# Performance work log

Measured on AMD Instinct MI355X. Metric: run time of the kernel, lower is better.

Reference implementation:

```python
import jax, jax.numpy as jnp
import numpy as np

H, BS, NB, R, K = 2048, 128, 44, 64, 8   # hidden, block_size, num_blocks, basis_rank, top_k
B, S = 4, 2048
I = NB * BS                               # intermediate size = 5632


def setup_inputs() -> dict:
    key = jax.random.key(0)
    ks = jax.random.split(key, 10)
    N = B * S
    return {
        "hidden_states": jax.random.normal(ks[0], (B, S, H), jnp.float32),
        "active_idx": jax.random.randint(ks[1], (N, K), 0, NB, jnp.int32),
        "active_score": jax.random.uniform(ks[2], (N, K), dtype=jnp.float32),
        "gate_w": jax.random.normal(ks[3], (I, H), jnp.float32) * 0.02,
        "up_w": jax.random.normal(ks[4], (I, H), jnp.float32) * 0.02,
        "down_w": jax.random.normal(ks[5], (H, I), jnp.float32) * 0.02,
        "enc_w": jax.random.normal(ks[6], (R, H), jnp.float32) * 0.02,
        "enc_b": jnp.zeros((R,), jnp.float32),
        "decoder": jax.random.normal(ks[7], (NB, R, BS), jnp.float32) * 0.02,
        "basis_bias": jnp.zeros((NB, BS), jnp.float32),
        "comp_bias": jnp.zeros((H,), jnp.float32),
        "scale": jnp.array(1.0, jnp.float32),
    }


def reference(hidden_states, active_idx, active_score, gate_w, up_w, down_w,
              enc_w, enc_b, decoder, basis_bias, comp_bias, scale):
    Bb, Ss, Hh = hidden_states.shape
    N = Bb * Ss
    x = hidden_states.reshape(N, Hh)                          # [N, H]

    # routing weights: softmax over selected block scores (all idx valid here),
    # scattered into a dense per-token per-block weight map (duplicates accumulate)
    w = jax.nn.softmax(active_score, axis=-1)                 # [N, K]
    block_w = jnp.zeros((N, NB), x.dtype).at[
        jnp.arange(N)[:, None], active_idx].add(w)            # [N, NB]

    # gated SiLU MLP intermediate over all blocks (dense equivalent of the
    # per-token block gather-compute)
    act = jax.nn.silu(x @ gate_w.T) * (x @ up_w.T)            # [N, I]

    # low-rank basis compensation: latent -> per-block block_size channels
    latent = jax.nn.silu(x @ enc_w.T + enc_b)                 # [N, R]
    comp = jnp.einsum('nr,brc->nbc', latent, decoder) + basis_bias  # [N, NB, BS]

    act_b = act.reshape(N, NB, BS) + scale * comp             # [N, NB, BS]
    weighted = (act_b * block_w[:, :, None]).reshape(N, I)    # mask+weight inactive blocks to 0

    out = weighted @ down_w.T + comp_bias                     # scatter back via down proj
    return out.reshape(Bb, Ss, Hh)
```

## Files before the change

### kernel.cpp

```cpp
#include <hip/hip_runtime.h>
#include <hip/hip_cooperative_groups.h>

namespace cg = cooperative_groups;

#define H_  2048
#define BS_ 128
#define NB_ 44
#define R_  64
#define K_  8
#define N_  8192
#define I_  5632
#define MT  64
#define TILES 32
#define DOWN_GRID 512
#define HC  512
#define MT2 128
#define TILES_GU 16
#define GRID_GU (8 * 6 * TILES_GU)

typedef __bf16 bf16x8 __attribute__((ext_vector_type(8)));
typedef float  f32x4  __attribute__((ext_vector_type(4)));

__device__ __forceinline__ unsigned short f2bf(float f) {
  unsigned int u = __float_as_uint(f);
  u = (u + 0x7FFFu + ((u >> 16) & 1u)) >> 16;
  return (unsigned short)u;
}
__device__ __forceinline__ bf16x8 ld8(const unsigned short* p) {
  uint4 v = *reinterpret_cast<const uint4*>(p);
  return __builtin_bit_cast(bf16x8, v);
}
__device__ __forceinline__ bf16x8 lds8(const char* p) {
  uint4 v = *reinterpret_cast<const uint4*>(p);
  return __builtin_bit_cast(bf16x8, v);
}
__device__ __forceinline__ void gl16(const void* g, void* l) {
  __builtin_amdgcn_global_load_lds(
      (const __attribute__((address_space(1))) char*)g,
      (__attribute__((address_space(3))) char*)l, 16, 0, 0);
}
#define WAIT_VM(n) do { asm volatile("s_waitcnt vmcnt(" #n ")" ::: "memory"); \
                        __builtin_amdgcn_sched_barrier(0); } while (0)
#define WAIT_LGKM0 do { asm volatile("s_waitcnt lgkmcnt(0)" ::: "memory"); \
                        __builtin_amdgcn_sched_barrier(0); } while (0)
#define SBAR __builtin_amdgcn_s_barrier()

__global__ void cvt_xgu(const float* __restrict__ x, const float* __restrict__ gw,
                        const float* __restrict__ uw, const float* __restrict__ ew,
                        const float* __restrict__ dw,
                        unsigned short* __restrict__ xb,
                        unsigned short* __restrict__ gwb,
                        unsigned short* __restrict__ uwb,
                        unsigned short* __restrict__ ewb,
                        unsigned short* __restrict__ dwb) {
  const int NX4 = N_ * H_ / 4;
  const int NG4 = I_ * H_ / 4;
  const int NE4 = R_ * H_ / 4;
  const int ND4 = H_ * I_ / 4;
  int total = NX4 + 2 * NG4 + NE4 + ND4;
  int stride = gridDim.x * blockDim.x;
  for (int i = blockIdx.x * blockDim.x + threadIdx.x; i < total; i += stride) {
    if (i < NX4 + 2 * NG4 + NE4) {
      const float4* s; ushort4* d; int j;
      if (i < NX4)                  { s = (const float4*)x;  d = (ushort4*)xb;  j = i; }
      else if (i < NX4 + NG4)       { s = (const float4*)gw; d = (ushort4*)gwb; j = i - NX4; }
      else if (i < NX4 + 2 * NG4)   { s = (const float4*)uw; d = (ushort4*)uwb; j = i - NX4 - NG4; }
      else                          { s = (const float4*)ew; d = (ushort4*)ewb; j = i - NX4 - 2 * NG4; }
      float4 v = s[j];
      ushort4 o; o.x = f2bf(v.x); o.y = f2bf(v.y); o.z = f2bf(v.z); o.w = f2bf(v.w);
      d[j] = o;
    } else {
      int j = i - (NX4 + 2 * NG4 + NE4);
      float4 v = ((const float4*)dw)[j];
      int flat = j * 4;
      int h = flat / I_;
      int rem = flat - h * I_;
      int b = rem >> 7, k = rem & 127;
      ushort4 o; o.x = f2bf(v.x); o.y = f2bf(v.y); o.z = f2bf(v.z); o.w = f2bf(v.w);
      *(ushort4*)(dwb + ((size_t)b * H_ + h) * BS_ + k) = o;
    }
  }
}

__global__ void cvt_dec(const float* __restrict__ dec, unsigned short* __restrict__ decb) {
  int i = blockIdx.x * 256 + threadIdx.x;
  if (i >= NB_ * BS_ * R_) return;
  int b = i >> 13;
  int rem = i & 8191;
  int c = rem >> 6, r = rem & 63;
  decb[i] = f2bf(dec[(b << 13) + r * BS_ + c]);
}

__global__ void zero_counts(int* __restrict__ counts) {
  if (threadIdx.x < NB_) counts[threadIdx.x] = 0;
}

__global__ void prep_kernel(const float* __restrict__ score,
                            const int* __restrict__ aidx,
                            float* __restrict__ w_buf,
                            int* __restrict__ counts) {
  __shared__ int hist[NB_];
  int tid = threadIdx.x;
  if (tid < NB_) hist[tid] = 0;
  __syncthreads();
  int n = blockIdx.x * 256 + tid;
  float s[K_];
  float m = -1e30f;
#pragma unroll
  for (int k = 0; k < K_; k++) { s[k] = score[n * K_ + k]; m = fmaxf(m, s[k]); }
  float sum = 0.f;
#pragma unroll
  for (int k = 0; k < K_; k++) { s[k] = __expf(s[k] - m); sum += s[k]; }
  float inv = 1.f / sum;
#pragma unroll
  for (int k = 0; k < K_; k++) {
    w_buf[n * K_ + k] = s[k] * inv;
    atomicAdd(&hist[aidx[n * K_ + k]], 1);
  }
  __syncthreads();
  if (tid < NB_) atomicAdd(&counts[tid], hist[tid]);
}

__global__ void scan_kernel(const int* __restrict__ counts,
                            int* __restrict__ offsets,
                            int* __restrict__ cursors) {
  if (threadIdx.x == 0) {
    int acc = 0;
    for (int b = 0; b < NB_; b++) { offsets[b] = acc; cursors[b] = acc; acc += counts[b]; }
    offsets[NB_] = acc;
  }
}

__global__ void fill_kernel(const int* __restrict__ aidx,
                            const float* __restrict__ w_buf,
                            int* __restrict__ cursors,
                            int* __restrict__ tok_list,
                            float* __restrict__ wt_list,
                            int* __restrict__ inv) {
  int n = blockIdx.x * 256 + threadIdx.x;
#pragma unroll
  for (int k = 0; k < K_; k++) {
    int b = aidx[n * K_ + k];
    int pos = atomicAdd(&cursors[b], 1);
    tok_list[pos] = n;
    wt_list[pos] = w_buf[n * K_ + k];
    inv[n * K_ + k] = pos;
  }
}

__global__ __launch_bounds__(256) void latent_mfma(
    const unsigned short* __restrict__ xb,
    const unsigned short* __restrict__ ewb,
    float* __restrict__ lat_part) {
  __shared__ __align__(16) char smem[16384];
  int tid = threadIdx.x;
  int wv = tid >> 6, lane = tid & 63;
  int lo = lane & 15, hi = lane >> 4;
  int grp = blockIdx.x >> 2, ksl = blockIdx.x & 3;
  int n0 = grp * 64;
  int k0 = ksl * 512;

  int rowA = tid >> 2;
  int jA = (tid & 3) ^ ((rowA >> 1) & 3);
  const unsigned short* srcA = xb + (size_t)(n0 + rowA) * H_ + k0 + jA * 8;
  const unsigned short* srcB = ewb + (size_t)rowA * H_ + k0 + jA * 8;

  gl16(srcA, smem + wv * 1024);
  gl16(srcB, smem + 8192 + wv * 1024);

  f32x4 acc[4] = {};
  int cur = 0;
  for (int ks = 0; ks < 512; ks += 32) {
    if (ks + 32 < 512) {
      gl16(srcA + ks + 32, smem + (cur ^ 1) * 4096 + wv * 1024);
      gl16(srcB + ks + 32, smem + 8192 + (cur ^ 1) * 4096 + wv * 1024);
      WAIT_VM(2);
    } else {
      WAIT_VM(0);
    }
    SBAR;
    int rB = wv * 16 + lo;
    bf16x8 Bf = lds8(smem + 8192 + cur * 4096 + (rB * 4 + (hi ^ ((rB >> 1) & 3))) * 16);
#pragma unroll
    for (int m = 0; m < 4; m++) {
      int row = m * 16 + lo;
      bf16x8 Af = lds8(smem + cur * 4096 + (row * 4 + (hi ^ ((row >> 1) & 3))) * 16);
      acc[m] = __builtin_amdgcn_mfma_f32_16x16x32_bf16(Af, Bf, acc[m], 0, 0, 0);
    }
    WAIT_LGKM0;
    SBAR;
    cur ^= 1;
  }

  int r = wv * 16 + lo;
  float* dst = lat_part + (size_t)ksl * N_ * R_;
#pragma unroll
  for (int m = 0; m < 4; m++) {
#pragma unroll
    for (int rg = 0; rg < 4; rg++) {
      int tok = n0 + m * 16 + hi * 4 + rg;
      dst[(size_t)tok * R_ + r] = acc[m][rg];
    }
  }
}

__global__ void latent_combine(const float* __restrict__ lp,
                               const float* __restrict__ enc_b,
                               unsigned short* __restrict__ lat) {
  const int T = N_ * R_;
  int i = blockIdx.x * 256 + threadIdx.x;
  if (i >= T) return;
  float v = lp[i] + lp[T + i] + lp[2 * T + i] + lp[3 * T + i] + enc_b[i & (R_ - 1)];
  lat[i] = f2bf(v / (1.f + __expf(-v)));
}

__device__ __forceinline__ bool decode_bt(int p, int& b, int& tile) {
  b = (p & 7) + 8 * ((p >> 3) / TILES);
  tile = (p >> 3) % TILES;
  return b < NB_;
}
__device__ __forceinline__ bool decode_bt_gu(int p, int& b, int& tile) {
  b = (p & 7) + 8 * ((p >> 3) / TILES_GU);
  tile = (p >> 3) % TILES_GU;
  return b < NB_;
}

__global__ __launch_bounds__(512, 4) void gateup_kernel(
    const unsigned short* __restrict__ xb,
    const unsigned short* __restrict__ gwb,
    const unsigned short* __restrict__ uwb,
    const unsigned short* __restrict__ latb,
    const unsigned short* __restrict__ decb_all,
    const float* __restrict__ bbias,
    const float* __restrict__ scale_p,
    const int* __restrict__ counts,
    const int* __restrict__ offsets,
    const int* __restrict__ tok_list,
    const float* __restrict__ wt_list,
    unsigned short* __restrict__ actw) {
  int b, tile;
  if (!decode_bt_gu(blockIdx.x, b, tile)) return;
  int cnt = counts[b];
  int base = tile * MT2;
  if (base >= cnt) return;
  int off = offsets[b];

  __shared__ __align__(16) char smem[49152];

  int tid = threadIdx.x;
  int wv = tid >> 6, lane = tid & 63;
  int lo = lane & 15, hi = lane >> 4;
  int wr = wv >> 2, wc = wv & 3;

  int rowA = tid >> 2;
  int jA = (tid & 3) ^ ((rowA >> 1) & 3);
  int tokA = tok_list[off + min(base + rowA, cnt - 1)];
  const unsigned short* srcA = xb + (size_t)tokA * H_ + jA * 8;

  const unsigned short* gb = gwb + (size_t)b * BS_ * H_;
  const unsigned short* ub = uwb + (size_t)b * BS_ * H_;
  int cS = tid >> 2;
  int jS = (tid & 3) ^ ((cS >> 1) & 3);
  const unsigned short* srcG = gb + (size_t)cS * H_ + jS * 8;
  const unsigned short* srcU = ub + (size_t)cS * H_ + jS * 8;

  f32x4 accG[4][2] = {};
  f32x4 accU[4][2] = {};

  gl16(srcA, smem + wv * 1024);
  gl16(srcG, smem + 16384 + wv * 1024);
  gl16(srcU, smem + 32768 + wv * 1024);

  for (int it = 0; it < 64; ++it) {
    int ks = it * 32;
    if (it < 63) {
      int nb_ = (it + 1) & 1;
      gl16(srcA + ks + 32, smem + nb_ * 8192 + wv * 1024);
      gl16(srcG + ks + 32, smem + 16384 + nb_ * 8192 + wv * 1024);
      gl16(srcU + ks + 32, smem + 32768 + nb_ * 8192 + wv * 1024);
      WAIT_VM(3);
    } else {
      WAIT_VM(0);
    }
    SBAR;
    int cur = it & 1;
    bf16x8 Af[4];
#pragma unroll
    for (int m = 0; m < 4; m++) {
      int row = wr * 64 + m * 16 + lo;
      int off16 = row * 4 + (hi ^ ((row >> 1) & 3));
      Af[m] = lds8(smem + cur * 8192 + off16 * 16);
    }
    bf16x8 Gf[2], Uf[2];
#pragma unroll
    for (int cf = 0; cf < 2; cf++) {
      int c = wc * 32 + cf * 16 + lo;
      int off16 = c * 4 + (hi ^ ((c >> 1) & 3));
      Gf[cf] = lds8(smem + 16384 + cur * 8192 + off16 * 16);
      Uf[cf] = lds8(smem + 32768 + cur * 8192 + off16 * 16);
    }
#pragma unroll
    for (int m = 0; m < 4; m++) {
#pragma unroll
      for (int cf = 0; cf < 2; cf++) {
        accG[m][cf] = __builtin_amdgcn_mfma_f32_16x16x32_bf16(Af[m], Gf[cf], accG[m][cf], 0, 0, 0);
        accU[m][cf] = __builtin_amdgcn_mfma_f32_16x16x32_bf16(Af[m], Uf[cf], accU[m][cf], 0, 0, 0);
      }
    }
    WAIT_LGKM0;
    SBAR;
  }

#pragma unroll
  for (int s = 0; s < 2; s++) {
    int o = s * 512 + tid;
    int r_ = o >> 3;
    int j = (o & 7) ^ (r_ & 7);
    int tokL = tok_list[off + min(base + r_, cnt - 1)];
    gl16(latb + (size_t)tokL * R_ + j * 8, smem + 32768 + s * 8192 + wv * 1024);
  }
  const unsigned short* decb = decb_all + (size_t)b * BS_ * R_;
#pragma unroll
  for (int s = 0; s < 2; s++) {
    int o = s * 512 + tid;
    int c = o >> 3;
    int j = (o & 7) ^ (c & 7);
    gl16(decb + (size_t)c * R_ + j * 8, smem + 16384 + s * 8192 + wv * 1024);
  }
  __syncthreads();

  f32x4 accC[4][2] = {};
#pragma unroll
  for (int kk = 0; kk < 2; kk++) {
    bf16x8 L[4];
#pragma unroll
    for (int m = 0; m < 4; m++) {
      int row = wr * 64 + m * 16 + lo;
      int off16 = row * 8 + ((kk * 4 + hi) ^ (row & 7));
      L[m] = lds8(smem + 32768 + off16 * 16);
    }
#pragma unroll
    for (int cf = 0; cf < 2; cf++) {
      int c = wc * 32 + cf * 16 + lo;
      int off16 = c * 8 + ((kk * 4 + hi) ^ (c & 7));
      bf16x8 D = lds8(smem + 16384 + off16 * 16);
#pragma unroll
      for (int m = 0; m < 4; m++)
        accC[m][cf] = __builtin_amdgcn_mfma_f32_16x16x32_bf16(L[m], D, accC[m][cf], 0, 0, 0);
    }
  }

  float scal = scale_p[0];
  int cc[2] = { wc * 32 + lo, wc * 32 + 16 + lo };
  float bbv[2] = { bbias[b * BS_ + cc[0]], bbias[b * BS_ + cc[1]] };
#pragma unroll
  for (int m = 0; m < 4; m++) {
#pragma unroll
    for (int r = 0; r < 4; r++) {
      int t = wr * 64 + m * 16 + hi * 4 + r;
      int g = base + t;
      if (g < cnt) {
        float wt = wt_list[off + g];
        unsigned short* dst = actw + (size_t)(off + g) * BS_;
#pragma unroll
        for (int cf = 0; cf < 2; cf++) {
          float gg = accG[m][cf][r];
          float uu = accU[m][cf][r];
          float act = (gg / (1.f + __expf(-gg))) * uu;
          dst[cc[cf]] = f2bf((act + scal * (accC[m][cf][r] + bbv[cf])) * wt);
        }
      }
    }
  }
}

__global__ __launch_bounds__(256) void downred_kernel(
    const unsigned short* __restrict__ actw,
    const unsigned short* __restrict__ dwb,
    const int* __restrict__ counts,
    const int* __restrict__ offsets,
    const int* __restrict__ inv,
    const float* __restrict__ cbias,
    unsigned short* __restrict__ partial,
    float* __restrict__ out) {
  cg::grid_group grid = cg::this_grid();
  __shared__ __align__(16) unsigned short a_lds[MT * BS_];
  __shared__ __align__(16) char b_lds[2][16384];
  int tid = threadIdx.x;
  int wv = tid >> 6, lane = tid & 63;
  int lo = lane & 15, hi = lane >> 4;
  int rs = tid >> 4;
  int jc = tid & 15;

  for (int c = 0; c < H_ / HC; c++) {
    int hc0 = c * HC;
    unsigned short* pchunk = partial + (size_t)c * 65536 * HC;

    for (int p = blockIdx.x; p < 8 * 6 * TILES; p += DOWN_GRID) {
      int b, tile;
      if (!decode_bt(p, b, tile)) continue;
      int cnt = counts[b];
      int base = tile * MT;
      if (base >= cnt) continue;
      int off = offsets[b];

      for (int i = tid; i < MT * BS_ / 8; i += 256) {
        int t = i >> 4, cb = i & 15;
        int g = base + t;
        uint4 v = make_uint4(0, 0, 0, 0);
        if (g < cnt) v = *(const uint4*)(actw + (size_t)(off + g) * BS_ + cb * 8);
        *(uint4*)(&a_lds[t * BS_ + ((cb ^ (t & 7)) << 3)]) = v;
      }
      __syncthreads();

      bf16x8 Bf[4][4];
#pragma unroll
      for (int kst = 0; kst < 4; kst++)
#pragma unroll
        for (int sf = 0; sf < 4; sf++) {
          int t = sf * 16 + lo, cb = kst * 4 + hi;
          Bf[kst][sf] = ld8(&a_lds[t * BS_ + ((cb ^ (t & 7)) << 3)]);
        }

      const unsigned short* db = dwb + (size_t)b * H_ * BS_;
      {
        const unsigned short* d0 = db + (size_t)hc0 * BS_;
#pragma unroll
        for (int s = 0; s < 4; s++) {
          int r = s * 16 + rs;
          int j = jc ^ (r & 15);
          gl16(d0 + (size_t)r * BS_ + j * 8, b_lds[0] + s * 4096 + wv * 1024);
        }
      }
      __syncthreads();

      int cur = 0;
      for (int it = 0; it < HC / 64; it++) {
        if (it + 1 < HC / 64) {
          const unsigned short* dn = db + (size_t)(hc0 + (it + 1) * 64) * BS_;
#pragma unroll
          for (int s = 0; s < 4; s++) {
            int r = s * 16 + rs;
            int j = jc ^ (r & 15);
            gl16(dn + (size_t)r * BS_ + j * 8, b_lds[cur ^ 1] + s * 4096 + wv * 1024);
          }
        }
        f32x4 acc[4] = {};
        int rl = wv * 16 + lo;
#pragma unroll
        for (int kst = 0; kst < 4; kst++) {
          int cb = kst * 4 + hi;
          bf16x8 Aw = lds8(b_lds[cur] + (rl * 16 + (cb ^ lo)) * 16);
#pragma unroll
          for (int sf = 0; sf < 4; sf++)
            acc[sf] = __builtin_amdgcn_mfma_f32_16x16x32_bf16(Aw, Bf[kst][sf], acc[sf], 0, 0, 0);
        }
        int hrel = it * 64 + wv * 16 + hi * 4;
#pragma unroll
        for (int sf = 0; sf < 4; sf++) {
          int g = base + sf * 16 + lo;
          if (g < cnt) {
            uint2 pk;
            pk.x = (unsigned int)f2bf(acc[sf][0]) | ((unsigned int)f2bf(acc[sf][1]) << 16);
            pk.y = (unsigned int)f2bf(acc[sf][2]) | ((unsigned int)f2bf(acc[sf][3]) << 16);
            *(uint2*)(pchunk + (size_t)(off + g) * HC + hrel) = pk;
          }
        }
        __syncthreads();
        cur ^= 1;
      }
    }

    grid.sync();

    for (int n = blockIdx.x * 4 + wv; n < N_; n += DOWN_GRID * 4) {
      int rows[K_];
#pragma unroll
      for (int k = 0; k < K_; k++) rows[k] = inv[n * K_ + k];
      int cw = lane * 8;
      float a[8] = {0.f, 0.f, 0.f, 0.f, 0.f, 0.f, 0.f, 0.f};
#pragma unroll
      for (int k = 0; k < K_; k++) {
        uint4 v = *(const uint4*)(pchunk + (size_t)rows[k] * HC + cw);
        unsigned int w0 = v.x, w1 = v.y, w2 = v.z, w3 = v.w;
        a[0] += __uint_as_float(w0 << 16); a[1] += __uint_as_float(w0 & 0xFFFF0000u);
        a[2] += __uint_as_float(w1 << 16); a[3] += __uint_as_float(w1 & 0xFFFF0000u);
        a[4] += __uint_as_float(w2 << 16); a[5] += __uint_as_float(w2 & 0xFFFF0000u);
        a[6] += __uint_as_float(w3 << 16); a[7] += __uint_as_float(w3 & 0xFFFF0000u);
      }
      int h = hc0 + cw;
      float4 c0 = *(const float4*)(cbias + h);
      float4 c1 = *(const float4*)(cbias + h + 4);
      float4 o0 = make_float4(a[0] + c0.x, a[1] + c0.y, a[2] + c0.z, a[3] + c0.w);
      float4 o1 = make_float4(a[4] + c1.x, a[5] + c1.y, a[6] + c1.z, a[7] + c1.w);
      *(float4*)(out + (size_t)n * H_ + h) = o0;
      *(float4*)(out + (size_t)n * H_ + h + 4) = o1;
    }

    grid.sync();
  }
}

__global__ __launch_bounds__(256) void down_kernel(
    const unsigned short* __restrict__ actw,
    const unsigned short* __restrict__ dwb,
    const int* __restrict__ counts,
    const int* __restrict__ offsets,
    unsigned short* __restrict__ partial,
    int hc0) {
  __shared__ __align__(16) unsigned short a_lds[MT * BS_];
  __shared__ __align__(16) char b_lds[2][16384];
  int tid = threadIdx.x;
  int wv = tid >> 6, lane = tid & 63;
  int lo = lane & 15, hi = lane >> 4;
  int rs = tid >> 4;
  int jc = tid & 15;

  for (int p = blockIdx.x; p < 8 * 6 * TILES; p += DOWN_GRID) {
    int b, tile;
    if (!decode_bt(p, b, tile)) continue;
    int cnt = counts[b];
    int base = tile * MT;
    if (base >= cnt) continue;
    int off = offsets[b];

    for (int i = tid; i < MT * BS_ / 8; i += 256) {
      int t = i >> 4, cb = i & 15;
      int g = base + t;
      uint4 v = make_uint4(0, 0, 0, 0);
      if (g < cnt) v = *(const uint4*)(actw + (size_t)(off + g) * BS_ + cb * 8);
      *(uint4*)(&a_lds[t * BS_ + ((cb ^ (t & 7)) << 3)]) = v;
    }
    __syncthreads();

    bf16x8 Bf[4][4];
#pragma unroll
    for (int kst = 0; kst < 4; kst++)
#pragma unroll
      for (int sf = 0; sf < 4; sf++) {
        int t = sf * 16 + lo, cb = kst * 4 + hi;
        Bf[kst][sf] = ld8(&a_lds[t * BS_ + ((cb ^ (t & 7)) << 3)]);
      }

    const unsigned short* db = dwb + (size_t)b * H_ * BS_;
    {
      const unsigned short* d0 = db + (size_t)hc0 * BS_;
#pragma unroll
      for (int s = 0; s < 4; s++) {
        int r = s * 16 + rs;
        int j = jc ^ (r & 15);
        gl16(d0 + (size_t)r * BS_ + j * 8, b_lds[0] + s * 4096 + wv * 1024);
      }
    }
    __syncthreads();

    int cur = 0;
    for (int it = 0; it < HC / 64; it++) {
      if (it + 1 < HC / 64) {
        const unsigned short* dn = db + (size_t)(hc0 + (it + 1) * 64) * BS_;
#pragma unroll
        for (int s = 0; s < 4; s++) {
          int r = s * 16 + rs;
          int j = jc ^ (r & 15);
          gl16(dn + (size_t)r * BS_ + j * 8, b_lds[cur ^ 1] + s * 4096 + wv * 1024);
        }
      }
      f32x4 acc[4] = {};
      int rl = wv * 16 + lo;
#pragma unroll
      for (int kst = 0; kst < 4; kst++) {
        int cb = kst * 4 + hi;
        bf16x8 Aw = lds8(b_lds[cur] + (rl * 16 + (cb ^ lo)) * 16);
#pragma unroll
        for (int sf = 0; sf < 4; sf++)
          acc[sf] = __builtin_amdgcn_mfma_f32_16x16x32_bf16(Aw, Bf[kst][sf], acc[sf], 0, 0, 0);
      }
      int hrel = it * 64 + wv * 16 + hi * 4;
#pragma unroll
      for (int sf = 0; sf < 4; sf++) {
        int g = base + sf * 16 + lo;
        if (g < cnt) {
          uint2 pk;
          pk.x = (unsigned int)f2bf(acc[sf][0]) | ((unsigned int)f2bf(acc[sf][1]) << 16);
          pk.y = (unsigned int)f2bf(acc[sf][2]) | ((unsigned int)f2bf(acc[sf][3]) << 16);
          *(uint2*)(partial + (size_t)(off + g) * HC + hrel) = pk;
        }
      }
      __syncthreads();
      cur ^= 1;
    }
  }
}

__global__ __launch_bounds__(256) void reduce_kernel(
    const unsigned short* __restrict__ partial,
    const int* __restrict__ inv,
    const float* __restrict__ cbias,
    float* __restrict__ out, int hc0) {
  int wv = threadIdx.x >> 6, l = threadIdx.x & 63;
  int n = blockIdx.x * 4 + wv;
  int rows[K_];
#pragma unroll
  for (int k = 0; k < K_; k++) rows[k] = inv[n * K_ + k];
  int cw = l * 8;
  float a[8] = {0.f, 0.f, 0.f, 0.f, 0.f, 0.f, 0.f, 0.f};
#pragma unroll
  for (int k = 0; k < K_; k++) {
    uint4 v = *(const uint4*)(partial + (size_t)rows[k] * HC + cw);
    unsigned int w0 = v.x, w1 = v.y, w2 = v.z, w3 = v.w;
    a[0] += __uint_as_float(w0 << 16); a[1] += __uint_as_float(w0 & 0xFFFF0000u);
    a[2] += __uint_as_float(w1 << 16); a[3] += __uint_as_float(w1 & 0xFFFF0000u);
    a[4] += __uint_as_float(w2 << 16); a[5] += __uint_as_float(w2 & 0xFFFF0000u);
    a[6] += __uint_as_float(w3 << 16); a[7] += __uint_as_float(w3 & 0xFFFF0000u);
  }
  int h = hc0 + cw;
  float4 c0 = *(const float4*)(cbias + h);
  float4 c1 = *(const float4*)(cbias + h + 4);
  float4 o0 = make_float4(a[0] + c0.x, a[1] + c0.y, a[2] + c0.z, a[3] + c0.w);
  float4 o1 = make_float4(a[4] + c1.x, a[5] + c1.y, a[6] + c1.z, a[7] + c1.w);
  *(float4*)(out + (size_t)n * H_ + h) = o0;
  *(float4*)(out + (size_t)n * H_ + h + 4) = o1;
}

extern "C" void kernel_launch(void* const* d_in, const int* in_sizes, int n_in,
                              void* d_out, int out_size, void* d_ws, size_t ws_size,
                              hipStream_t stream) {
  const float* x       = (const float*)d_in[0];
  const int*   aidx    = (const int*)d_in[1];
  const float* score   = (const float*)d_in[2];
  const float* gate_w  = (const float*)d_in[3];
  const float* up_w    = (const float*)d_in[4];
  const float* down_w  = (const float*)d_in[5];
  const float* enc_w   = (const float*)d_in[6];
  const float* enc_b   = (const float*)d_in[7];
  const float* decoder = (const float*)d_in[8];
  const float* bbias   = (const float*)d_in[9];
  const float* cbias   = (const float*)d_in[10];
  const float* scale   = (const float*)d_in[11];
  float* out = (float*)d_out;

  char* ws = (char*)d_ws;
  const size_t OFF_GWB  = 33554432ull;
  const size_t OFF_UWB  = 56623104ull;
  const size_t OFF_DEC  = 79691776ull;
  const size_t OFF_LATB = 80412672ull;
  const size_t OFF_ENCB = 81461248ull;
  const size_t OFF_WBUF = 81723392ull;
  const size_t OFF_TOK  = 81985536ull;
  const size_t OFF_WT   = 82247680ull;
  const size_t OFF_INV  = 82509824ull;
  const size_t OFF_CNT  = 82771968ull;
  const size_t OFF_ACTW = 82772992ull;
  const size_t BASE_END = 99550208ull;
  const size_t DWB_SZ   = 23068672ull;
  const size_t PART_FULL = 268435456ull;

  unsigned short* xb   = (unsigned short*)(ws);
  unsigned short* gwb  = (unsigned short*)(ws + OFF_GWB);
  unsigned short* uwb  = (unsigned short*)(ws + OFF_UWB);
  unsigned short* decb = (unsigned short*)(ws + OFF_DEC);
  unsigned short* latb = (unsigned short*)(ws + OFF_LATB);
  unsigned short* ewb  = (unsigned short*)(ws + OFF_ENCB);
  float* w_buf         = (float*)(ws + OFF_WBUF);
  int*   tok_list      = (int*)(ws + OFF_TOK);
  float* wt_list       = (float*)(ws + OFF_WT);
  int*   inv           = (int*)(ws + OFF_INV);
  int*   counts        = (int*)(ws + OFF_CNT);
  int*   offsets       = counts + 64;
  int*   cursors       = counts + 128;
  unsigned short* actw = (unsigned short*)(ws + OFF_ACTW);

  unsigned short* dwb     = (unsigned short*)(ws + BASE_END);
  unsigned short* partial = (unsigned short*)(ws + BASE_END + DWB_SZ);
  float* lat_part         = (float*)(ws + BASE_END + DWB_SZ);

  bool full = ws_size >= BASE_END + DWB_SZ + PART_FULL;

  cvt_xgu<<<2048, 256, 0, stream>>>(x, gate_w, up_w, enc_w, down_w,
                                    xb, gwb, uwb, ewb, dwb);
  cvt_dec<<<(NB_ * BS_ * R_ + 255) / 256, 256, 0, stream>>>(decoder, decb);
  zero_counts<<<1, 64, 0, stream>>>(counts);
  prep_kernel<<<N_ / 256, 256, 0, stream>>>(score, aidx, w_buf, counts);
  scan_kernel<<<1, 64, 0, stream>>>(counts, offsets, cursors);
  fill_kernel<<<N_ / 256, 256, 0, stream>>>(aidx, w_buf, cursors, tok_list, wt_list, inv);
  latent_mfma<<<N_ / 16, 256, 0, stream>>>(xb, ewb, lat_part);
  latent_combine<<<N_ * R_ / 256, 256, 0, stream>>>(lat_part, enc_b, latb);
  gateup_kernel<<<GRID_GU, 512, 0, stream>>>(xb, gwb, uwb, latb, decb, bbias, scale,
                                             counts, offsets, tok_list, wt_list, actw);

  bool coop_done = false;
  if (full) {
    void* args[] = { (void*)&actw, (void*)&dwb, (void*)&counts, (void*)&offsets,
                     (void*)&inv, (void*)&cbias, (void*)&partial, (void*)&out };
    hipError_t rc = hipLaunchCooperativeKernel((const void*)downred_kernel,
                                               dim3(DOWN_GRID), dim3(256),
                                               args, 0, stream);
    coop_done = (rc == hipSuccess);
  }
  if (!coop_done) {
    for (int c = 0; c < H_ / HC; c++) {
      down_kernel<<<DOWN_GRID, 256, 0, stream>>>(actw, dwb, counts, offsets, partial, c * HC);
      reduce_kernel<<<N_ / 4, 256, 0, stream>>>(partial, inv, cbias, out, c * HC);
    }
  }
}
```

Measured before the change: 538.3 us.

## Fuse front-end conversion, routing, latent and gate-up into one cooperative kernel

Replaces the chain of small launches (conversion, prep, scan, fill, latent matmul plus combine, gate-up) with a single cooperative kernel that uses grid.sync between phases. The latent matmul now does its full K reduction per block with the bias and SiLU fused in, so the split-K partial buffer and the combine kernel go away. This removes launch overhead and intermediate round trips. The price is that the grid is limited to GRID_GU blocks of 512 threads with 48KB of LDS, which may lower parallelism in the conversion phase and cost occupancy. The old launch sequence is kept as a fallback if the cooperative launch fails.

```diff
diff --git a/kernel.cpp b/kernel.cpp
--- a/kernel.cpp
+++ b/kernel.cpp
@@ -17,6 +17,7 @@
 #define MT2 128
 #define TILES_GU 16
 #define GRID_GU (8 * 6 * TILES_GU)
+#define FRONT_GRID GRID_GU
 
 typedef __bf16 bf16x8 __attribute__((ext_vector_type(8)));
 typedef float  f32x4  __attribute__((ext_vector_type(4)));
@@ -44,6 +45,425 @@
 #define WAIT_LGKM0 do { asm volatile("s_waitcnt lgkmcnt(0)" ::: "memory"); \
                         __builtin_amdgcn_sched_barrier(0); } while (0)
 #define SBAR __builtin_amdgcn_s_barrier()
+
+__device__ __forceinline__ bool decode_bt(int p, int& b, int& tile) {
+  b = (p & 7) + 8 * ((p >> 3) / TILES);
+  tile = (p >> 3) % TILES;
+  return b < NB_;
+}
+__device__ __forceinline__ bool decode_bt_gu(int p, int& b, int& tile) {
+  b = (p & 7) + 8 * ((p >> 3) / TILES_GU);
+  tile = (p >> 3) % TILES_GU;
+  return b < NB_;
+}
+
+__global__ __launch_bounds__(512, 6) void front_kernel(
+    const float* __restrict__ x, const float* __restrict__ gw,
+    const float* __restrict__ uw, const float* __restrict__ ew,
+    const float* __restrict__ dw, const float* __restrict__ dec,
+    const float* __restrict__ score, const int* __restrict__ aidx,
+    const float* __restrict__ enc_b, const float* __restrict__ bbias,
+    const float* __restrict__ scale_p,
+    unsigned short* __restrict__ xb, unsigned short* __restrict__ gwb,
+    unsigned short* __restrict__ uwb, unsigned short* __restrict__ ewb,
+    unsigned short* __restrict__ dwb, unsigned short* __restrict__ decb_all,
+    unsigned short* __restrict__ latb,
+    float* __restrict__ w_buf, int* __restrict__ counts,
+    int* __restrict__ offsets, int* __restrict__ cursors,
+    int* __restrict__ tok_list, float* __restrict__ wt_list,
+    int* __restrict__ inv, unsigned short* __restrict__ actw) {
+  cg::grid_group grid = cg::this_grid();
+  __shared__ __align__(16) char smem[49152];
+  int tid = threadIdx.x;
+  int bId = blockIdx.x;
+
+  if (bId < 16) {
+    int* hist = (int*)smem;
+    if (tid < NB_) hist[tid] = 0;
+    __syncthreads();
+    int n = bId * 512 + tid;
+    float s[K_];
+    float m = -1e30f;
+#pragma unroll
+    for (int k = 0; k < K_; k++) { s[k] = score[n * K_ + k]; m = fmaxf(m, s[k]); }
+    float sum = 0.f;
+#pragma unroll
+    for (int k = 0; k < K_; k++) { s[k] = __expf(s[k] - m); sum += s[k]; }
+    float is = 1.f / sum;
+#pragma unroll
+    for (int k = 0; k < K_; k++) {
+      w_buf[n * K_ + k] = s[k] * is;
+      atomicAdd(&hist[aidx[n * K_ + k]], 1);
+    }
+    __syncthreads();
+    if (tid < NB_) atomicAdd(&counts[tid], hist[tid]);
+  }
+
+  {
+    const int NX4 = N_ * H_ / 4;
+    const int NG4 = I_ * H_ / 4;
+    const int NE4 = R_ * H_ / 4;
+    const int ND4 = H_ * I_ / 4;
+    int total = NX4 + 2 * NG4 + NE4 + ND4;
+    int stride = FRONT_GRID * 512;
+    for (int i = bId * 512 + tid; i < total; i += stride) {
+      if (i < NX4 + 2 * NG4 + NE4) {
+        const float4* s; ushort4* d; int j;
+        if (i < NX4)                { s = (const float4*)x;  d = (ushort4*)xb;  j = i; }
+        else if (i < NX4 + NG4)     { s = (const float4*)gw; d = (ushort4*)gwb; j = i - NX4; }
+        else if (i < NX4 + 2 * NG4) { s = (const float4*)uw; d = (ushort4*)uwb; j = i - NX4 - NG4; }
+        else                        { s = (const float4*)ew; d = (ushort4*)ewb; j = i - NX4 - 2 * NG4; }
+        float4 v = s[j];
+        ushort4 o; o.x = f2bf(v.x); o.y = f2bf(v.y); o.z = f2bf(v.z); o.w = f2bf(v.w);
+        d[j] = o;
+      } else {
+        int j = i - (NX4 + 2 * NG4 + NE4);
+        float4 v = ((const float4*)dw)[j];
+        int flat = j * 4;
+        int h = flat / I_;
+        int rem = flat - h * I_;
+        int b = rem >> 7, k = rem & 127;
+        ushort4 o; o.x = f2bf(v.x); o.y = f2bf(v.y); o.z = f2bf(v.z); o.w = f2bf(v.w);
+        *(ushort4*)(dwb + ((size_t)b * H_ + h) * BS_ + k) = o;
+      }
+    }
+    for (int i = bId * 512 + tid; i < NB_ * BS_ * R_; i += stride) {
+      int b = i >> 13;
+      int rem = i & 8191;
+      int c = rem >> 6, r = rem & 63;
+      decb_all[i] = f2bf(dec[(b << 13) + r * BS_ + c]);
+    }
+  }
+  grid.sync();
+
+  if (bId == 0 && tid == 0) {
+    int acc = 0;
+    for (int b = 0; b < NB_; b++) { offsets[b] = acc; cursors[b] = acc; acc += counts[b]; }
+    offsets[NB_] = acc;
+  }
+  grid.sync();
+
+  if (bId < 16) {
+    int n = bId * 512 + tid;
+#pragma unroll
+    for (int k = 0; k < K_; k++) {
+      int b = aidx[n * K_ + k];
+      int pos = atomicAdd(&cursors[b], 1);
+      tok_list[pos] = n;
+      wt_list[pos] = w_buf[n * K_ + k];
+      inv[n * K_ + k] = pos;
+    }
+  } else if (bId < 80) {
+    int g = tid >> 8;
+    int t = tid & 255;
+    int wvg = t >> 6;
+    int lane = t & 63, lo = lane & 15, hi = lane >> 4;
+    int n0 = (bId - 16) * 128 + g * 64;
+    char* sm = smem + g * 16384;
+    int rowA = t >> 2;
+    int jA = (t & 3) ^ ((rowA >> 1) & 3);
+    const unsigned short* srcA = xb + (size_t)(n0 + rowA) * H_ + jA * 8;
+    const unsigned short* srcB = ewb + (size_t)rowA * H_ + jA * 8;
+    gl16(srcA, sm + wvg * 1024);
+    gl16(srcB, sm + 8192 + wvg * 1024);
+    f32x4 acc[4] = {};
+    int cur = 0;
+    for (int ks = 0; ks < H_; ks += 32) {
+      if (ks + 32 < H_) {
+        gl16(srcA + ks + 32, sm + (cur ^ 1) * 4096 + wvg * 1024);
+        gl16(srcB + ks + 32, sm + 8192 + (cur ^ 1) * 4096 + wvg * 1024);
+        WAIT_VM(2);
+      } else {
+        WAIT_VM(0);
+      }
+      SBAR;
+      int rB = wvg * 16 + lo;
+      bf16x8 Bf = lds8(sm + 8192 + cur * 4096 + (rB * 4 + (hi ^ ((rB >> 1) & 3))) * 16);
+#pragma unroll
+      for (int m = 0; m < 4; m++) {
+        int row = m * 16 + lo;
+        bf16x8 Af = lds8(sm + cur * 4096 + (row * 4 + (hi ^ ((row >> 1) & 3))) * 16);
+        acc[m] = __builtin_amdgcn_mfma_f32_16x16x32_bf16(Af, Bf, acc[m], 0, 0, 0);
+      }
+      WAIT_LGKM0;
+      SBAR;
+      cur ^= 1;
+    }
+    int r = wvg * 16 + lo;
+    float eb = enc_b[r];
+#pragma unroll
+    for (int m = 0; m < 4; m++) {
+#pragma unroll
+      for (int rg = 0; rg < 4; rg++) {
+        int tok = n0 + m * 16 + hi * 4 + rg;
+        float v = acc[m][rg] + eb;
+        latb[(size_t)tok * R_ + r] = f2bf(v / (1.f + __expf(-v)));
+      }
+    }
+  }
+  grid.sync();
+
+  {
+    int b, tile;
+    if (!decode_bt_gu(bId, b, tile)) return;
+    int cnt = counts[b];
+    int base = tile * MT2;
+    if (base >= cnt) return;
+    int off = offsets[b];
+
+    int wv = tid >> 6, lane = tid & 63;
+    int lo = lane & 15, hi = lane >> 4;
+    int wr = wv >> 2, wc = wv & 3;
+
+    int rowA = tid >> 2;
+    int jA = (tid & 3) ^ ((rowA >> 1) & 3);
+    int tokA = tok_list[off + min(base + rowA, cnt - 1)];
+    const unsigned short* srcA = xb + (size_t)tokA * H_ + jA * 8;
+
+    const unsigned short* gb = gwb + (size_t)b * BS_ * H_;
+    const unsigned short* ub = uwb + (size_t)b * BS_ * H_;
+    int cS = tid >> 2;
+    int jS = (tid & 3) ^ ((cS >> 1) & 3);
+    const unsigned short* srcG = gb + (size_t)cS * H_ + jS * 8;
+    const unsigned short* srcU = ub + (size_t)cS * H_ + jS * 8;
+
+    f32x4 accG[4][2] = {};
+    f32x4 accU[4][2] = {};
+
+    gl16(srcA, smem + wv * 1024);
+    gl16(srcG, smem + 16384 + wv * 1024);
+    gl16(srcU, smem + 32768 + wv * 1024);
+
+    for (int it = 0; it < 64; ++it) {
+      int ks = it * 32;
+      if (it < 63) {
+        int nb_ = (it + 1) & 1;
+        gl16(srcA + ks + 32, smem + nb_ * 8192 + wv * 1024);
+        gl16(srcG + ks + 32, smem + 16384 + nb_ * 8192 + wv * 1024);
+        gl16(srcU + ks + 32, smem + 32768 + nb_ * 8192 + wv * 1024);
+        WAIT_VM(3);
+      } else {
+        WAIT_VM(0);
+      }
+      SBAR;
+      int cur = it & 1;
+      bf16x8 Af[4];
+#pragma unroll
+      for (int m = 0; m < 4; m++) {
+        int row = wr * 64 + m * 16 + lo;
+        int off16 = row * 4 + (hi ^ ((row >> 1) & 3));
+        Af[m] = lds8(smem + cur * 8192 + off16 * 16);
+      }
+      bf16x8 Gf[2], Uf[2];
+#pragma unroll
+      for (int cf = 0; cf < 2; cf++) {
+        int c = wc * 32 + cf * 16 + lo;
+        int off16 = c * 4 + (hi ^ ((c >> 1) & 3));
+        Gf[cf] = lds8(smem + 16384 + cur * 8192 + off16 * 16);
+        Uf[cf] = lds8(smem + 32768 + cur * 8192 + off16 * 16);
+      }
+#pragma unroll
+      for (int m = 0; m < 4; m++) {
+#pragma unroll
+        for (int cf = 0; cf < 2; cf++) {
+          accG[m][cf] = __builtin_amdgcn_mfma_f32_16x16x32_bf16(Af[m], Gf[cf], accG[m][cf], 0, 0, 0);
+          accU[m][cf] = __builtin_amdgcn_mfma_f32_16x16x32_bf16(Af[m], Uf[cf], accU[m][cf], 0, 0, 0);
+        }
+      }
+      WAIT_LGKM0;
+      SBAR;
+    }
+
+#pragma unroll
+    for (int s = 0; s < 2; s++) {
+      int o = s * 512 + tid;
+      int r_ = o >> 3;
+      int j = (o & 7) ^ (r_ & 7);
+      int tokL = tok_list[off + min(base + r_, cnt - 1)];
+      gl16(latb + (size_t)tokL * R_ + j * 8, smem + 32768 + s * 8192 + wv * 1024);
+    }
+    const unsigned short* decb = decb_all + (size_t)b * BS_ * R_;
+#pragma unroll
+    for (int s = 0; s < 2; s++) {
+      int o = s * 512 + tid;
+      int c = o >> 3;
+      int j = (o & 7) ^ (c & 7);
+      gl16(decb + (size_t)c * R_ + j * 8, smem + 16384 + s * 8192 + wv * 1024);
+    }
+    __syncthreads();
+
+    f32x4 accC[4][2] = {};
+#pragma unroll
+    for (int kk = 0; kk < 2; kk++) {
+      bf16x8 L[4];
+#pragma unroll
+      for (int m = 0; m < 4; m++) {
+        int row = wr * 64 + m * 16 + lo;
+        int off16 = row * 8 + ((kk * 4 + hi) ^ (row & 7));
+        L[m] = lds8(smem + 32768 + off16 * 16);
+      }
+#pragma unroll
+      for (int cf = 0; cf < 2; cf++) {
+        int c = wc * 32 + cf * 16 + lo;
+        int off16 = c * 8 + ((kk * 4 + hi) ^ (c & 7));
+        bf16x8 D = lds8(smem + 16384 + off16 * 16);
+#pragma unroll
+        for (int m = 0; m < 4; m++)
+          accC[m][cf] = __builtin_amdgcn_mfma_f32_16x16x32_bf16(L[m], D, accC[m][cf], 0, 0, 0);
+      }
+    }
+
+    float scal = scale_p[0];
+    int cc[2] = { wc * 32 + lo, wc * 32 + 16 + lo };
+    float bbv[2] = { bbias[b * BS_ + cc[0]], bbias[b * BS_ + cc[1]] };
+#pragma unroll
+    for (int m = 0; m < 4; m++) {
+#pragma unroll
+      for (int r = 0; r < 4; r++) {
+        int t = wr * 64 + m * 16 + hi * 4 + r;
+        int g = base + t;
+        if (g < cnt) {
+          float wt = wt_list[off + g];
+          unsigned short* dst = actw + (size_t)(off + g) * BS_;
+#pragma unroll
+          for (int cf = 0; cf < 2; cf++) {
+            float gg = accG[m][cf][r];
+            float uu = accU[m][cf][r];
+            float act = (gg / (1.f + __expf(-gg))) * uu;
+            dst[cc[cf]] = f2bf((act + scal * (accC[m][cf][r] + bbv[cf])) * wt);
+          }
+        }
+      }
+    }
+  }
+}
+
+__global__ __launch_bounds__(256) void downred_kernel(
+    const unsigned short* __restrict__ actw,
+    const unsigned short* __restrict__ dwb,
+    const int* __restrict__ counts,
+    const int* __restrict__ offsets,
+    const int* __restrict__ inv,
+    const float* __restrict__ cbias,
+    unsigned short* __restrict__ partial,
+    float* __restrict__ out) {
+  cg::grid_group grid = cg::this_grid();
+  __shared__ __align__(16) unsigned short a_lds[MT * BS_];
+  __shared__ __align__(16) char b_lds[2][16384];
+  int tid = threadIdx.x;
+  int wv = tid >> 6, lane = tid & 63;
+  int lo = lane & 15, hi = lane >> 4;
+  int rs = tid >> 4;
+  int jc = tid & 15;
+
+  for (int c = 0; c < H_ / HC; c++) {
+    int hc0 = c * HC;
+    unsigned short* pchunk = partial + (size_t)c * 65536 * HC;
+
+    for (int p = blockIdx.x; p < 8 * 6 * TILES; p += DOWN_GRID) {
+      int b, tile;
+      if (!decode_bt(p, b, tile)) continue;
+      int cnt = counts[b];
+      int base = tile * MT;
+      if (base >= cnt) continue;
+      int off = offsets[b];
+
+      for (int i = tid; i < MT * BS_ / 8; i += 256) {
+        int t = i >> 4, cb = i & 15;
+        int g = base + t;
+        uint4 v = make_uint4(0, 0, 0, 0);
+        if (g < cnt) v = *(const uint4*)(actw + (size_t)(off + g) * BS_ + cb * 8);
+        *(uint4*)(&a_lds[t * BS_ + ((cb ^ (t & 7)) << 3)]) = v;
+      }
+      __syncthreads();
+
+      bf16x8 Bf[4][4];
+#pragma unroll
+      for (int kst = 0; kst < 4; kst++)
+#pragma unroll
+        for (int sf = 0; sf < 4; sf++) {
+          int t = sf * 16 + lo, cb = kst * 4 + hi;
+          Bf[kst][sf] = ld8(&a_lds[t * BS_ + ((cb ^ (t & 7)) << 3)]);
+        }
+
+      const unsigned short* db = dwb + (size_t)b * H_ * BS_;
+      {
+        const unsigned short* d0 = db + (size_t)hc0 * BS_;
+#pragma unroll
+        for (int s = 0; s < 4; s++) {
+          int r = s * 16 + rs;
+          int j = jc ^ (r & 15);
+          gl16(d0 + (size_t)r * BS_ + j * 8, b_lds[0] + s * 4096 + wv * 1024);
+        }
+      }
+      __syncthreads();
+
+      int cur = 0;
+      for (int it = 0; it < HC / 64; it++) {
+        if (it + 1 < HC / 64) {
+          const unsigned short* dn = db + (size_t)(hc0 + (it + 1) * 64) * BS_;
+#pragma unroll
+          for (int s = 0; s < 4; s++) {
+            int r = s * 16 + rs;
+            int j = jc ^ (r & 15);
+            gl16(dn + (size_t)r * BS_ + j * 8, b_lds[cur ^ 1] + s * 4096 + wv * 1024);
+          }
+        }
+        f32x4 acc[4] = {};
+        int rl = wv * 16 + lo;
+#pragma unroll
+        for (int kst = 0; kst < 4; kst++) {
+          int cb = kst * 4 + hi;
+          bf16x8 Aw = lds8(b_lds[cur] + (rl * 16 + (cb ^ lo)) * 16);
+#pragma unroll
+          for (int sf = 0; sf < 4; sf++)
+            acc[sf] = __builtin_amdgcn_mfma_f32_16x16x32_bf16(Aw, Bf[kst][sf], acc[sf], 0, 0, 0);
+        }
+        int hrel = it * 64 + wv * 16 + hi * 4;
+#pragma unroll
+        for (int sf = 0; sf < 4; sf++) {
+          int g = base + sf * 16 + lo;
+          if (g < cnt) {
+            uint2 pk;
+            pk.x = (unsigned int)f2bf(acc[sf][0]) | ((unsigned int)f2bf(acc[sf][1]) << 16);
+            pk.y = (unsigned int)f2bf(acc[sf][2]) | ((unsigned int)f2bf(acc[sf][3]) << 16);
+            *(uint2*)(pchunk + (size_t)(off + g) * HC + hrel) = pk;
+          }
+        }
+        __syncthreads();
+        cur ^= 1;
+      }
+    }
+
+    grid.sync();
+
+    for (int n = blockIdx.x * 4 + wv; n < N_; n += DOWN_GRID * 4) {
+      int rows[K_];
+#pragma unroll
+      for (int k = 0; k < K_; k++) rows[k] = inv[n * K_ + k];
+      int cw = lane * 8;
+      float a[8] = {0.f, 0.f, 0.f, 0.f, 0.f, 0.f, 0.f, 0.f};
+#pragma unroll
+      for (int k = 0; k < K_; k++) {
+        uint4 v = *(const uint4*)(pchunk + (size_t)rows[k] * HC + cw);
+        unsigned int w0 = v.x, w1 = v.y, w2 = v.z, w3 = v.w;
+        a[0] += __uint_as_float(w0 << 16); a[1] += __uint_as_float(w0 & 0xFFFF0000u);
+        a[2] += __uint_as_float(w1 << 16); a[3] += __uint_as_float(w1 & 0xFFFF0000u);
+        a[4] += __uint_as_float(w2 << 16); a[5] += __uint_as_float(w2 & 0xFFFF0000u);
+        a[6] += __uint_as_float(w3 << 16); a[7] += __uint_as_float(w3 & 0xFFFF0000u);
+      }
+      int h = hc0 + cw;
+      float4 c0 = *(const float4*)(cbias + h);
+      float4 c1 = *(const float4*)(cbias + h + 4);
+      float4 o0 = make_float4(a[0] + c0.x, a[1] + c0.y, a[2] + c0.z, a[3] + c0.w);
+      float4 o1 = make_float4(a[4] + c1.x, a[5] + c1.y, a[6] + c1.z, a[7] + c1.w);
+      *(float4*)(out + (size_t)n * H_ + h) = o0;
+      *(float4*)(out + (size_t)n * H_ + h + 4) = o1;
+    }
+
+    grid.sync();
+  }
+}
 
 __global__ void cvt_xgu(const float* __restrict__ x, const float* __restrict__ gw,
                         const float* __restrict__ uw, const float* __restrict__ ew,
@@ -62,10 +482,10 @@
   for (int i = blockIdx.x * blockDim.x + threadIdx.x; i < total; i += stride) {
     if (i < NX4 + 2 * NG4 + NE4) {
       const float4* s; ushort4* d; int j;
-      if (i < NX4)                  { s = (const float4*)x;  d = (ushort4*)xb;  j = i; }
-      else if (i < NX4 + NG4)       { s = (const float4*)gw; d = (ushort4*)gwb; j = i - NX4; }
-      else if (i < NX4 + 2 * NG4)   { s = (const float4*)uw; d = (ushort4*)uwb; j = i - NX4 - NG4; }
-      else                          { s = (const float4*)ew; d = (ushort4*)ewb; j = i - NX4 - 2 * NG4; }
+      if (i < NX4)                { s = (const float4*)x;  d = (ushort4*)xb;  j = i; }
+      else if (i < NX4 + NG4)     { s = (const float4*)gw; d = (ushort4*)gwb; j = i - NX4; }
+      else if (i < NX4 + 2 * NG4) { s = (const float4*)uw; d = (ushort4*)uwb; j = i - NX4 - NG4; }
+      else                        { s = (const float4*)ew; d = (ushort4*)ewb; j = i - NX4 - 2 * NG4; }
       float4 v = s[j];
       ushort4 o; o.x = f2bf(v.x); o.y = f2bf(v.y); o.z = f2bf(v.z); o.w = f2bf(v.w);
       d[j] = o;
@@ -91,10 +511,6 @@
   decb[i] = f2bf(dec[(b << 13) + r * BS_ + c]);
 }
 
-__global__ void zero_counts(int* __restrict__ counts) {
-  if (threadIdx.x < NB_) counts[threadIdx.x] = 0;
-}
-
 __global__ void prep_kernel(const float* __restrict__ score,
                             const int* __restrict__ aidx,
                             float* __restrict__ w_buf,
@@ -111,10 +527,10 @@
   float sum = 0.f;
 #pragma unroll
   for (int k = 0; k < K_; k++) { s[k] = __expf(s[k] - m); sum += s[k]; }
-  float inv = 1.f / sum;
+  float is = 1.f / sum;
 #pragma unroll
   for (int k = 0; k < K_; k++) {
-    w_buf[n * K_ + k] = s[k] * inv;
+    w_buf[n * K_ + k] = s[k] * is;
     atomicAdd(&hist[aidx[n * K_ + k]], 1);
   }
   __syncthreads();
@@ -148,30 +564,29 @@
   }
 }
 
-__global__ __launch_bounds__(256) void latent_mfma(
+__global__ __launch_bounds__(256) void latent_fb(
     const unsigned short* __restrict__ xb,
     const unsigned short* __restrict__ ewb,
-    float* __restrict__ lat_part) {
+    const float* __restrict__ enc_b,
+    unsigned short* __restrict__ lat) {
   __shared__ __align__(16) char smem[16384];
   int tid = threadIdx.x;
   int wv = tid >> 6, lane = tid & 63;
   int lo = lane & 15, hi = lane >> 4;
-  int grp = blockIdx.x >> 2, ksl = blockIdx.x & 3;
-  int n0 = grp * 64;
-  int k0 = ksl * 512;
+  int n0 = blockIdx.x * 64;
 
   int rowA = tid >> 2;
   int jA = (tid & 3) ^ ((rowA >> 1) & 3);
-  const unsigned short* srcA = xb + (size_t)(n0 + rowA) * H_ + k0 + jA * 8;
-  const unsigned short* srcB = ewb + (size_t)rowA * H_ + k0 + jA * 8;
+  const unsigned short* srcA = xb + (size_t)(n0 + rowA) * H_ + jA * 8;
+  const unsigned short* srcB = ewb + (size_t)rowA * H_ + jA * 8;
 
   gl16(srcA, smem + wv * 1024);
   gl16(srcB, smem + 8192 + wv * 1024);
 
   f32x4 acc[4] = {};
   int cur = 0;
-  for (int ks = 0; ks < 512; ks += 32) {
-    if (ks + 32 < 512) {
+  for (int ks = 0; ks < H_; ks += 32) {
+    if (ks + 32 < H_) {
       gl16(srcA + ks + 32, smem + (cur ^ 1) * 4096 + wv * 1024);
       gl16(srcB + ks + 32, smem + 8192 + (cur ^ 1) * 4096 + wv * 1024);
       WAIT_VM(2);
@@ -193,36 +608,16 @@
   }
 
   int r = wv * 16 + lo;
-  float* dst = lat_part + (size_t)ksl * N_ * R_;
+  float eb = enc_b[r];
 #pragma unroll
   for (int m = 0; m < 4; m++) {
 #pragma unroll
     for (int rg = 0; rg < 4; rg++) {
       int tok = n0 + m * 16 + hi * 4 + rg;
-      dst[(size_t)tok * R_ + r] = acc[m][rg];
-    }
-  }
-}
-
-__global__ void latent_combine(const float* __restrict__ lp,
-                               const float* __restrict__ enc_b,
-                               unsigned short* __restrict__ lat) {
-  const int T = N_ * R_;
-  int i = blockIdx.x * 256 + threadIdx.x;
-  if (i >= T) return;
-  float v = lp[i] + lp[T + i] + lp[2 * T + i] + lp[3 * T + i] + enc_b[i & (R_ - 1)];
-  lat[i] = f2bf(v / (1.f + __expf(-v)));
-}
-
-__device__ __forceinline__ bool decode_bt(int p, int& b, int& tile) {
-  b = (p & 7) + 8 * ((p >> 3) / TILES);
-  tile = (p >> 3) % TILES;
-  return b < NB_;
-}
-__device__ __forceinline__ bool decode_bt_gu(int p, int& b, int& tile) {
-  b = (p & 7) + 8 * ((p >> 3) / TILES_GU);
-  tile = (p >> 3) % TILES_GU;
-  return b < NB_;
+      float v = acc[m][rg] + eb;
+      lat[(size_t)tok * R_ + r] = f2bf(v / (1.f + __expf(-v)));
+    }
+  }
 }
 
 __global__ __launch_bounds__(512, 4) void gateup_kernel(
@@ -374,133 +769,6 @@
   }
 }
 
-__global__ __launch_bounds__(256) void downred_kernel(
-    const unsigned short* __restrict__ actw,
-    const unsigned short* __restrict__ dwb,
-    const int* __restrict__ counts,
-    const int* __restrict__ offsets,
-    const int* __restrict__ inv,
-    const float* __restrict__ cbias,
-    unsigned short* __restrict__ partial,
-    float* __restrict__ out) {
-  cg::grid_group grid = cg::this_grid();
-  __shared__ __align__(16) unsigned short a_lds[MT * BS_];
-  __shared__ __align__(16) char b_lds[2][16384];
-  int tid = threadIdx.x;
-  int wv = tid >> 6, lane = tid & 63;
-  int lo = lane & 15, hi = lane >> 4;
-  int rs = tid >> 4;
-  int jc = tid & 15;
-
-  for (int c = 0; c < H_ / HC; c++) {
-    int hc0 = c * HC;
-    unsigned short* pchunk = partial + (size_t)c * 65536 * HC;
-
-    for (int p = blockIdx.x; p < 8 * 6 * TILES; p += DOWN_GRID) {
-      int b, tile;
-      if (!decode_bt(p, b, tile)) continue;
-      int cnt = counts[b];
-      int base = tile * MT;
-      if (base >= cnt) continue;
-      int off = offsets[b];
-
-      for (int i = tid; i < MT * BS_ / 8; i += 256) {
-        int t = i >> 4, cb = i & 15;
-        int g = base + t;
-        uint4 v = make_uint4(0, 0, 0, 0);
-        if (g < cnt) v = *(const uint4*)(actw + (size_t)(off + g) * BS_ + cb * 8);
-        *(uint4*)(&a_lds[t * BS_ + ((cb ^ (t & 7)) << 3)]) = v;
-      }
-      __syncthreads();
-
-      bf16x8 Bf[4][4];
-#pragma unroll
-      for (int kst = 0; kst < 4; kst++)
-#pragma unroll
-        for (int sf = 0; sf < 4; sf++) {
-          int t = sf * 16 + lo, cb = kst * 4 + hi;
-          Bf[kst][sf] = ld8(&a_lds[t * BS_ + ((cb ^ (t & 7)) << 3)]);
-        }
-
-      const unsigned short* db = dwb + (size_t)b * H_ * BS_;
-      {
-        const unsigned short* d0 = db + (size_t)hc0 * BS_;
-#pragma unroll
-        for (int s = 0; s < 4; s++) {
-          int r = s * 16 + rs;
-          int j = jc ^ (r & 15);
-          gl16(d0 + (size_t)r * BS_ + j * 8, b_lds[0] + s * 4096 + wv * 1024);
-        }
-      }
-      __syncthreads();
-
-      int cur = 0;
-      for (int it = 0; it < HC / 64; it++) {
-        if (it + 1 < HC / 64) {
-          const unsigned short* dn = db + (size_t)(hc0 + (it + 1) * 64) * BS_;
-#pragma unroll
-          for (int s = 0; s < 4; s++) {
-            int r = s * 16 + rs;
-            int j = jc ^ (r & 15);
-            gl16(dn + (size_t)r * BS_ + j * 8, b_lds[cur ^ 1] + s * 4096 + wv * 1024);
-          }
-        }
-        f32x4 acc[4] = {};
-        int rl = wv * 16 + lo;
-#pragma unroll
-        for (int kst = 0; kst < 4; kst++) {
-          int cb = kst * 4 + hi;
-          bf16x8 Aw = lds8(b_lds[cur] + (rl * 16 + (cb ^ lo)) * 16);
-#pragma unroll
-          for (int sf = 0; sf < 4; sf++)
-            acc[sf] = __builtin_amdgcn_mfma_f32_16x16x32_bf16(Aw, Bf[kst][sf], acc[sf], 0, 0, 0);
-        }
-        int hrel = it * 64 + wv * 16 + hi * 4;
-#pragma unroll
-        for (int sf = 0; sf < 4; sf++) {
-          int g = base + sf * 16 + lo;
-          if (g < cnt) {
-            uint2 pk;
-            pk.x = (unsigned int)f2bf(acc[sf][0]) | ((unsigned int)f2bf(acc[sf][1]) << 16);
-            pk.y = (unsigned int)f2bf(acc[sf][2]) | ((unsigned int)f2bf(acc[sf][3]) << 16);
-            *(uint2*)(pchunk + (size_t)(off + g) * HC + hrel) = pk;
-          }
-        }
-        __syncthreads();
-        cur ^= 1;
-      }
-    }
-
-    grid.sync();
-
-    for (int n = blockIdx.x * 4 + wv; n < N_; n += DOWN_GRID * 4) {
-      int rows[K_];
-#pragma unroll
-      for (int k = 0; k < K_; k++) rows[k] = inv[n * K_ + k];
-      int cw = lane * 8;
-      float a[8] = {0.f, 0.f, 0.f, 0.f, 0.f, 0.f, 0.f, 0.f};
-#pragma unroll
-      for (int k = 0; k < K_; k++) {
-        uint4 v = *(const uint4*)(pchunk + (size_t)rows[k] * HC + cw);
-        unsigned int w0 = v.x, w1 = v.y, w2 = v.z, w3 = v.w;
-        a[0] += __uint_as_float(w0 << 16); a[1] += __uint_as_float(w0 & 0xFFFF0000u);
-        a[2] += __uint_as_float(w1 << 16); a[3] += __uint_as_float(w1 & 0xFFFF0000u);
-        a[4] += __uint_as_float(w2 << 16); a[5] += __uint_as_float(w2 & 0xFFFF0000u);
-        a[6] += __uint_as_float(w3 << 16); a[7] += __uint_as_float(w3 & 0xFFFF0000u);
-      }
-      int h = hc0 + cw;
-      float4 c0 = *(const float4*)(cbias + h);
-      float4 c1 = *(const float4*)(cbias + h + 4);
-      float4 o0 = make_float4(a[0] + c0.x, a[1] + c0.y, a[2] + c0.z, a[3] + c0.w);
-      float4 o1 = make_float4(a[4] + c1.x, a[5] + c1.y, a[6] + c1.z, a[7] + c1.w);
-      *(float4*)(out + (size_t)n * H_ + h) = o0;
-      *(float4*)(out + (size_t)n * H_ + h + 4) = o1;
-    }
-
-    grid.sync();
-  }
-}
-
 __global__ __launch_bounds__(256) void down_kernel(
     const unsigned short* __restrict__ actw,
     const unsigned short* __restrict__ dwb,
@@ -672,21 +940,36 @@
 
   unsigned short* dwb     = (unsigned short*)(ws + BASE_END);
   unsigned short* partial = (unsigned short*)(ws + BASE_END + DWB_SZ);
-  float* lat_part         = (float*)(ws + BASE_END + DWB_SZ);
 
   bool full = ws_size >= BASE_END + DWB_SZ + PART_FULL;
 
-  cvt_xgu<<<2048, 256, 0, stream>>>(x, gate_w, up_w, enc_w, down_w,
-                                    xb, gwb, uwb, ewb, dwb);
-  cvt_dec<<<(NB_ * BS_ * R_ + 255) / 256, 256, 0, stream>>>(decoder, decb);
-  zero_counts<<<1, 64, 0, stream>>>(counts);
-  prep_kernel<<<N_ / 256, 256, 0, stream>>>(score, aidx, w_buf, counts);
-  scan_kernel<<<1, 64, 0, stream>>>(counts, offsets, cursors);
-  fill_kernel<<<N_ / 256, 256, 0, stream>>>(aidx, w_buf, cursors, tok_list, wt_list, inv);
-  latent_mfma<<<N_ / 16, 256, 0, stream>>>(xb, ewb, lat_part);
-  latent_combine<<<N_ * R_ / 256, 256, 0, stream>>>(lat_part, enc_b, latb);
-  gateup_kernel<<<GRID_GU, 512, 0, stream>>>(xb, gwb, uwb, latb, decb, bbias, scale,
-                                             counts, offsets, tok_list, wt_list, actw);
+  hipMemsetAsync(counts, 0, 64 * sizeof(int), stream);
+
+  bool front_ok = false;
+  {
+    void* args[] = { (void*)&x, (void*)&gate_w, (void*)&up_w, (void*)&enc_w,
+                     (void*)&down_w, (void*)&decoder, (void*)&score, (void*)&aidx,
+                     (void*)&enc_b, (void*)&bbias, (void*)&scale,
+                     (void*)&xb, (void*)&gwb, (void*)&uwb, (void*)&ewb,
+                     (void*)&dwb, (void*)&decb, (void*)&latb,
+                     (void*)&w_buf, (void*)&counts, (void*)&offsets, (void*)&cursors,
+                     (void*)&tok_list, (void*)&wt_list, (void*)&inv, (void*)&actw };
+    hipError_t rc = hipLaunchCooperativeKernel((const void*)front_kernel,
+                                               dim3(FRONT_GRID), dim3(512),
+                                               args, 0, stream);
+    front_ok = (rc == hipSuccess);
+  }
+  if (!front_ok) {
+    cvt_xgu<<<2048, 256, 0, stream>>>(x, gate_w, up_w, enc_w, down_w,
+                                      xb, gwb, uwb, ewb, dwb);
+    cvt_dec<<<(NB_ * BS_ * R_ + 255) / 256, 256, 0, stream>>>(decoder, decb);
+    prep_kernel<<<N_ / 256, 256, 0, stream>>>(score, aidx, w_buf, counts);
+    scan_kernel<<<1, 64, 0, stream>>>(counts, offsets, cursors);
+    fill_kernel<<<N_ / 256, 256, 0, stream>>>(aidx, w_buf, cursors, tok_list, wt_list, inv);
+    latent_fb<<<N_ / 64, 256, 0, stream>>>(xb, ewb, enc_b, latb);
+    gateup_kernel<<<GRID_GU, 512, 0, stream>>>(xb, gwb, uwb, latb, decb, bbias, scale,
+                                               counts, offsets, tok_list, wt_list, actw);
+  }
 
   bool coop_done = false;
   if (full) {
```

Measured after the change: 1.372 ms. 2.55x slower.
